# Optimization experiments

Hardware: AMD Instinct MI355X
Metric: run time of the kernel (lower is better)

## Reference

```python
import jax, jax.numpy as jnp
import numpy as np

THRESHOLD = 0.5
NEG_POS_RATIO = 3
ALPHA = 1.0
B, A, C, M = 128, 8732, 21, 8


def cxcy_to_xy(c):
    return jnp.concatenate([c[:, :2] - c[:, 2:] / 2.0, c[:, :2] + c[:, 2:] / 2.0], axis=1)


def cxcy_to_gcxgcy(cxcy, priors):
    g_cxcy = (cxcy[:, :2] - priors[:, :2]) / (priors[:, 2:] / 10.0)
    g_wh = jnp.log(cxcy[:, 2:] / priors[:, 2:]) * 5.0
    return jnp.concatenate([g_cxcy, g_wh], axis=1)


def find_jaccard_overlap(a, b):
    # a: [M,4] xy, b: [A,4] xy -> IoU [M,A]
    lt = jnp.maximum(a[:, None, :2], b[None, :, :2])
    rb = jnp.minimum(a[:, None, 2:], b[None, :, 2:])
    wh = jnp.clip(rb - lt, 0.0)
    inter = wh[..., 0] * wh[..., 1]
    area_a = (a[:, 2] - a[:, 0]) * (a[:, 3] - a[:, 1])
    area_b = (b[:, 2] - b[:, 0]) * (b[:, 3] - b[:, 1])
    return inter / (area_a[:, None] + area_b[None, :] - inter)


def setup_inputs() -> dict:
    key = jax.random.key(0)
    k1, k2, k3, k4, k5, k6 = jax.random.split(key, 6)
    predicted_locs = jax.random.normal(k1, (B, A, 4), dtype=jnp.float32)
    predicted_scores = jax.random.normal(k2, (B, A, C), dtype=jnp.float32)
    # ground-truth boxes in xy pixel coords within [0, 300], guaranteed x2>x1, y2>y1
    u = jax.random.uniform(k3, (B, M, 4), dtype=jnp.float32)
    x1y1 = u[..., :2] * 150.0
    x2y2 = x1y1 + u[..., 2:] * 140.0 + 10.0
    boxes = jnp.concatenate([x1y1, x2y2], axis=-1)
    labels = jax.random.randint(k4, (B, M), 1, C)  # 1..20, never background
    # anchor boxes in cxcy, w/h strictly positive
    cxcy = jax.random.uniform(k5, (A, 2), dtype=jnp.float32)
    wh = 0.05 + 0.95 * jax.random.uniform(k6, (A, 2), dtype=jnp.float32)
    anchor_boxes = jnp.concatenate([cxcy, wh], axis=1)
    return {"predicted_locs": predicted_locs, "predicted_scores": predicted_scores,
            "boxes": boxes, "labels": labels, "anchor_boxes": anchor_boxes}


def _match(boxes_i, labels_i, anchors_cxcy, anchors_xy):
    # boxes_i: [M,4] xy pixels, labels_i: [M]
    scaled = boxes_i / 300.0
    iou = find_jaccard_overlap(scaled, anchors_xy)            # [M, A]
    obj_for_anchor = jnp.argmax(iou, axis=0)                  # [A]
    iou_for_anchor = jnp.max(iou, axis=0)                     # [A]
    anchor_for_obj = jnp.argmax(iou, axis=1)                  # [M]
    obj_for_anchor = obj_for_anchor.at[anchor_for_obj].set(jnp.arange(M))
    iou_for_anchor = iou_for_anchor.at[anchor_for_obj].set(1.0)
    label_for_anchor = labels_i[obj_for_anchor]               # [A]
    label_for_anchor = jnp.where(iou_for_anchor < THRESHOLD, 0, label_for_anchor)
    true_locs = cxcy_to_gcxgcy(boxes_i[obj_for_anchor], anchors_cxcy)  # [A,4]
    return label_for_anchor, true_locs


def reference(predicted_locs, predicted_scores, boxes, labels, anchor_boxes):
    anchors_xy = cxcy_to_xy(anchor_boxes)
    true_classes, true_locs = jax.vmap(_match, in_axes=(0, 0, None, None))(
        boxes, labels, anchor_boxes, anchors_xy)              # [B,A], [B,A,4]

    pos = true_classes != 0                                   # [B,A]
    n_pos = pos.sum(axis=1)                                   # [B]
    n_pos_total = n_pos.sum()

    # L1Loss(mean) over positive anchors' 4 coords
    l1 = jnp.abs(predicted_locs - true_locs)                  # [B,A,4]
    loc_loss = (l1 * pos[..., None]).sum() / (n_pos_total.astype(jnp.float32) * 4.0)

    # per-anchor cross entropy
    logp = jax.nn.log_softmax(predicted_scores, axis=-1)      # [B,A,C]
    ce = -jnp.take_along_axis(logp, true_classes[..., None], axis=-1)[..., 0]  # [B,A]

    conf_pos = (ce * pos).sum()
    ce_neg = jnp.where(pos, 0.0, ce)
    ce_neg_sorted = -jnp.sort(-ce_neg, axis=1)                # descending per row
    ranks = jnp.arange(A)[None, :]
    hard = ranks < (NEG_POS_RATIO * n_pos)[:, None]
    conf_hard_neg = (ce_neg_sorted * hard).sum()

    conf_loss = (conf_hard_neg + conf_pos) / n_pos_total.astype(jnp.float32)
    return conf_loss + ALPHA * loc_loss
```

## Files before the change

kernel.cpp:

```cpp
#include <hip/hip_runtime.h>
#include <hip/hip_bf16.h>

constexpr int B = 128;
constexpr int A = 8732;
constexpr int C = 21;
constexpr int M = 8;

__global__ void k_init(float* accf, int* npt) {
    int t = threadIdx.x;
    if (t < 3) accf[t] = 0.f;
    if (t == 3) *npt = 0;
}

__global__ __launch_bounds__(1024) void k_match(
    const float* __restrict__ boxes,
    const int*   __restrict__ labels,
    const float* __restrict__ anchors,
    int*         __restrict__ packed,
    int*         __restrict__ n_pos,
    int*         __restrict__ npt)
{
    __shared__ float         s_iou[A];
    __shared__ unsigned char s_obj[A];
    __shared__ float s_pv[M][16];
    __shared__ int   s_pi[M][16];
    __shared__ int   s_force[M];
    __shared__ int   s_c[16];
    __shared__ float s_box[M][4];
    __shared__ int   s_lab[M];

    const int b = blockIdx.x;
    const int t = threadIdx.x;
    const int lane = t & 63;
    const int wv   = t >> 6;

    if (t < M * 4) ((float*)s_box)[t] = boxes[b * M * 4 + t];
    if (t < M)     s_lab[t] = labels[b * M + t];
    __syncthreads();

    float bb[M][4], barea[M];
#pragma unroll
    for (int m = 0; m < M; m++) {
        bb[m][0] = s_box[m][0] / 300.f;
        bb[m][1] = s_box[m][1] / 300.f;
        bb[m][2] = s_box[m][2] / 300.f;
        bb[m][3] = s_box[m][3] / 300.f;
        barea[m] = (bb[m][2] - bb[m][0]) * (bb[m][3] - bb[m][1]);
    }

    float bestv[M];
    int   besti[M];
#pragma unroll
    for (int m = 0; m < M; m++) { bestv[m] = -1.f; besti[m] = 0; }

    const float4* anch4 = (const float4*)anchors;
    for (int a = t; a < A; a += 1024) {
        float4 an = anch4[a];
        float ax1 = an.x - an.z / 2.0f, ay1 = an.y - an.w / 2.0f;
        float ax2 = an.x + an.z / 2.0f, ay2 = an.y + an.w / 2.0f;
        float aarea = (ax2 - ax1) * (ay2 - ay1);

        float bmax = -1.f; int bm = 0;
#pragma unroll
        for (int m = 0; m < M; m++) {
            float lx = fmaxf(bb[m][0], ax1), ly = fmaxf(bb[m][1], ay1);
            float rx = fminf(bb[m][2], ax2), ry = fminf(bb[m][3], ay2);
            float iw = fmaxf(rx - lx, 0.f), ih = fmaxf(ry - ly, 0.f);
            float inter = iw * ih;
            float iou = inter / (barea[m] + aarea - inter);
            if (iou > bmax) { bmax = iou; bm = m; }
            if (iou > bestv[m]) { bestv[m] = iou; besti[m] = a; }
        }
        s_iou[a] = bmax;
        s_obj[a] = (unsigned char)bm;
    }

#pragma unroll
    for (int m = 0; m < M; m++) {
        float v = bestv[m]; int i = besti[m];
        for (int off = 32; off > 0; off >>= 1) {
            float ov = __shfl_down(v, off);
            int   oi = __shfl_down(i, off);
            if (ov > v || (ov == v && oi < i)) { v = ov; i = oi; }
        }
        if (lane == 0) { s_pv[m][wv] = v; s_pi[m][wv] = i; }
    }
    __syncthreads();

    if (t < M) {
        float bv = -1.f; int bi = 0x7fffffff;
#pragma unroll
        for (int w = 0; w < 16; w++) {
            float v = s_pv[t][w]; int i = s_pi[t][w];
            if (v > bv || (v == bv && i < bi)) { bv = v; bi = i; }
        }
        s_force[t] = bi;
    }
    __syncthreads();

    if (t == 0) {
        for (int m = 0; m < M; m++) {
            int a = s_force[m];
            s_obj[a] = (unsigned char)m;
            s_iou[a] = 1.0f;
        }
    }
    __syncthreads();

    int cnt = 0;
    for (int a = t; a < A; a += 1024) {
        int obj = s_obj[a];
        int lab = s_lab[obj];
        if (s_iou[a] < 0.5f) lab = 0;
        packed[(size_t)b * A + a] = lab | (obj << 8);
        if (lab != 0) cnt++;
    }
    for (int off = 32; off > 0; off >>= 1) cnt += __shfl_down(cnt, off);
    if (lane == 0) s_c[wv] = cnt;
    __syncthreads();
    if (t == 0) {
        int c0 = 0;
#pragma unroll
        for (int w = 0; w < 16; w++) c0 += s_c[w];
        n_pos[b] = c0;
        atomicAdd(npt, c0);
    }
}

__global__ __launch_bounds__(256) void k_ce(
    const float* __restrict__ plocs,
    const float* __restrict__ pscores,
    const float* __restrict__ boxes,
    const float* __restrict__ anchors,
    int*         __restrict__ buf,
    float*       __restrict__ accf)
{
    constexpr int NQ = B * A / 4;
    const int i4 = blockIdx.x * 256 + threadIdx.x;
    float l_pos = 0.f, l_loc = 0.f;

    if (i4 < NQ) {
        const int base = i4 * 4;
        const float4* s4 = (const float4*)(pscores + (size_t)base * C);
        float4 v[21];
#pragma unroll
        for (int i = 0; i < 21; i++) v[i] = s4[i];
        const float* f = (const float*)v;

        int4 pk4 = ((const int4*)buf)[i4];
        const int pks[4] = {pk4.x, pk4.y, pk4.z, pk4.w};

        const int b = base / A;
        const int a0 = base - b * A;

        float4 cn4;
        float* cn = (float*)&cn4;
#pragma unroll
        for (int j = 0; j < 4; j++) {
            const float* row = f + j * C;
            const int lab = pks[j] & 255;
            const int obj = pks[j] >> 8;

            float mx = row[0];
#pragma unroll
            for (int c = 1; c < C; c++) mx = fmaxf(mx, row[c]);
            float sum = 0.f, slab = 0.f;
#pragma unroll
            for (int c = 0; c < C; c++) {
                sum += __expf(row[c] - mx);
                if (c == lab) slab = row[c];
            }
            float ce = mx + __logf(sum) - slab;

            cn[j] = ce;
            if (lab != 0) {
                cn[j] = 0.f;
                l_pos += ce;
                const float* bx = boxes + ((size_t)b * M + obj) * 4;
                const float* an = anchors + (size_t)(a0 + j) * 4;
                float dx = (bx[0] - an[0]) / (an[2] / 10.f);
                float dy = (bx[1] - an[1]) / (an[3] / 10.f);
                float dw = logf(bx[2] / an[2]) * 5.f;
                float dh = logf(bx[3] / an[3]) * 5.f;
                float4 p = ((const float4*)plocs)[base + j];
                l_loc += fabsf(p.x - dx) + fabsf(p.y - dy) +
                         fabsf(p.z - dw) + fabsf(p.w - dh);
            }
        }
        ((float4*)buf)[i4] = cn4;
    }

    for (int off = 32; off > 0; off >>= 1) {
        l_pos += __shfl_down(l_pos, off);
        l_loc += __shfl_down(l_loc, off);
    }
    if ((threadIdx.x & 63) == 0 && (l_pos != 0.f || l_loc != 0.f)) {
        atomicAdd(&accf[0], l_pos);
        atomicAdd(&accf[1], l_loc);
    }
}

__global__ __launch_bounds__(1024) void k_topk(
    const float* __restrict__ ce_neg,
    const int*   __restrict__ n_pos,
    float*       __restrict__ accf)
{
    __shared__ unsigned int vals[A];
    __shared__ unsigned int hist[256];
    __shared__ unsigned int s_prefix, s_krem;
    __shared__ float        rs[16];
    __shared__ unsigned int rc[16];

    const int b = blockIdx.x;
    const int t = threadIdx.x;
    const int lane = t & 63;
    const int wv   = t >> 6;
    const int K = 3 * n_pos[b];
    const float* row = ce_neg + (size_t)b * A;

    {
        const uint4* r4 = (const uint4*)row;
        uint4* v4 = (uint4*)vals;
        for (int i = t; i < A / 4; i += 1024) v4[i] = r4[i];
    }
    if (t == 0) { s_prefix = 0u; s_krem = (unsigned)K; }
    __syncthreads();

    if (K <= 0) return;

    if (K >= A) {
        float s = 0.f;
        for (int i = t; i < A; i += 1024) s += __uint_as_float(vals[i]);
        for (int off = 32; off > 0; off >>= 1) s += __shfl_down(s, off);
        if (lane == 0) rs[wv] = s;
        __syncthreads();
        if (t == 0) {
            float tot = 0.f;
#pragma unroll
            for (int w = 0; w < 16; w++) tot += rs[w];
            atomicAdd(&accf[2], tot);
        }
        return;
    }

    for (int pass = 0; pass < 4; pass++) {
        const int shift = 24 - 8 * pass;
        const unsigned pref = s_prefix;
        const unsigned krem = s_krem;
        if (t < 256) hist[t] = 0u;
        __syncthreads();
        for (int i = t; i < A; i += 1024) {
            unsigned int v = vals[i];
            if (pass == 0 || (v >> (shift + 8)) == pref)
                atomicAdd(&hist[(v >> shift) & 255u], 1u);
        }
        __syncthreads();
        if (t < 64) {
            unsigned h0 = hist[4 * t + 0], h1 = hist[4 * t + 1];
            unsigned h2 = hist[4 * t + 2], h3 = hist[4 * t + 3];
            unsigned s3 = h3, s2 = h2 + s3, s1 = h1 + s2, s0 = h0 + s1;
            unsigned suf = s0;
            for (int off = 1; off < 64; off <<= 1) {
                unsigned o = __shfl_down(suf, off);
                if (t + off < 64) suf += o;
            }
            unsigned above = suf - s0;
            hist[4 * t + 0] = above + s0;
            hist[4 * t + 1] = above + s1;
            hist[4 * t + 2] = above + s2;
            hist[4 * t + 3] = above + s3;
        }
        __syncthreads();
        if (t < 256) {
            unsigned ssT = hist[t];
            unsigned ssN = (t < 255) ? hist[t + 1] : 0u;
            if (ssT >= krem && ssN < krem) {
                s_prefix = (pref << 8) | (unsigned)t;
                s_krem   = krem - ssN;
            }
        }
        __syncthreads();
    }

    const unsigned int tb = s_prefix;
    float sg = 0.f; unsigned int cg = 0;
    for (int i = t; i < A; i += 1024) {
        unsigned int v = vals[i];
        if (v > tb) { sg += __uint_as_float(v); cg++; }
    }
    for (int off = 32; off > 0; off >>= 1) {
        sg += __shfl_down(sg, off);
        cg += __shfl_down(cg, off);
    }
    if (lane == 0) { rs[wv] = sg; rc[wv] = cg; }
    __syncthreads();
    if (t == 0) {
        float tv = __uint_as_float(tb);
        float tot = 0.f; unsigned cnt = 0;
#pragma unroll
        for (int w = 0; w < 16; w++) { tot += rs[w]; cnt += rc[w]; }
        atomicAdd(&accf[2], tot + (float)(K - (int)cnt) * tv);
    }
}

__global__ void k_final(const float* __restrict__ accf,
                        const int* __restrict__ npt,
                        float* __restrict__ out)
{
    float n = (float)(*npt);
    float conf_loss = (accf[2] + accf[0]) / n;
    float loc_loss  = accf[1] / (n * 4.f);
    out[0] = conf_loss + loc_loss;
}

extern "C" void kernel_launch(void* const* d_in, const int* in_sizes, int n_in,
                              void* d_out, int out_size, void* d_ws, size_t ws_size,
                              hipStream_t stream)
{
    const float* plocs   = (const float*)d_in[0];
    const float* pscores = (const float*)d_in[1];
    const float* boxes   = (const float*)d_in[2];
    const int*   labels  = (const int*)d_in[3];
    const float* anchors = (const float*)d_in[4];
    float*       out     = (float*)d_out;

    float* accf  = (float*)d_ws;
    int*   npt   = (int*)d_ws + 3;
    int*   n_pos = (int*)d_ws + 8;
    int*   buf   = (int*)d_ws + 8 + B;

    k_init<<<1, 64, 0, stream>>>(accf, npt);
    k_match<<<B, 1024, 0, stream>>>(boxes, labels, anchors, buf, n_pos, npt);
    constexpr int NQ = B * A / 4;
    k_ce<<<(NQ + 255) / 256, 256, 0, stream>>>(plocs, pscores, boxes, anchors, buf, accf);
    k_topk<<<B, 1024, 0, stream>>>((const float*)buf, n_pos, accf);
    k_final<<<1, 1, 0, stream>>>(accf, npt, out);
}
```

Measured before the change: 287.8 us.

## Split anchor matching across slices and stage CE scores through double-buffered LDS

Matching now runs as 16 slices per image with 256-thread blocks instead of one 1024-thread block per image. Each slice writes its packed labels directly and publishes per-object best anchors through 64-bit atomicMax keys. A new small patch kernel then applies the forced matches and corrects the positive counts. The CE kernel becomes a persistent grid that streams 256-anchor chunks of scores with coalesced float4 loads into a double-buffered shared-memory tile, prefetching the next chunk while it computes. This trades an extra launch and global atomics for much higher parallelism in matching and better load coalescing in CE.

```diff
diff --git a/kernel.cpp b/kernel.cpp
--- a/kernel.cpp
+++ b/kernel.cpp
@@ -1,38 +1,51 @@
 #include <hip/hip_runtime.h>
-#include <hip/hip_bf16.h>
 
 constexpr int B = 128;
 constexpr int A = 8732;
 constexpr int C = 21;
 constexpr int M = 8;
-
-__global__ void k_init(float* accf, int* npt) {
+constexpr int S  = 16;
+constexpr int AS = (A + S - 1) / S;
+constexpr int CH = 256;
+constexpr int NCH = B * A / CH;
+constexpr int CE_GRID = 768;
+
+
+__global__ __launch_bounds__(256) void k_init(float* accf, int* npt, int* n_pos,
+                                              unsigned long long* keys) {
     int t = threadIdx.x;
     if (t < 3) accf[t] = 0.f;
     if (t == 3) *npt = 0;
-}
-
-__global__ __launch_bounds__(1024) void k_match(
+    if (t < B) n_pos[t] = 0;
+#pragma unroll
+    for (int k = 0; k < (B * M + 255) / 256; k++) {
+        int i = t + k * 256;
+        if (i < B * M) keys[i] = 0ull;
+    }
+}
+
+__global__ __launch_bounds__(256) void k_match_slice(
     const float* __restrict__ boxes,
     const int*   __restrict__ labels,
     const float* __restrict__ anchors,
     int*         __restrict__ packed,
     int*         __restrict__ n_pos,
-    int*         __restrict__ npt)
-{
-    __shared__ float         s_iou[A];
-    __shared__ unsigned char s_obj[A];
-    __shared__ float s_pv[M][16];
-    __shared__ int   s_pi[M][16];
-    __shared__ int   s_force[M];
-    __shared__ int   s_c[16];
+    unsigned long long* __restrict__ keys)
+{
     __shared__ float s_box[M][4];
     __shared__ int   s_lab[M];
-
-    const int b = blockIdx.x;
-    const int t = threadIdx.x;
+    __shared__ float s_pv[M][4];
+    __shared__ int   s_pi[M][4];
+    __shared__ int   s_c[4];
+
+    const int bs = blockIdx.x;
+    const int b  = bs >> 4;
+    const int s  = bs & (S - 1);
+    const int t  = threadIdx.x;
     const int lane = t & 63;
     const int wv   = t >> 6;
+    const int a_lo = s * AS;
+    const int a_hi = (a_lo + AS < A) ? a_lo + AS : A;
 
     if (t < M * 4) ((float*)s_box)[t] = boxes[b * M * 4 + t];
     if (t < M)     s_lab[t] = labels[b * M + t];
@@ -51,10 +64,11 @@
     float bestv[M];
     int   besti[M];
 #pragma unroll
-    for (int m = 0; m < M; m++) { bestv[m] = -1.f; besti[m] = 0; }
+    for (int m = 0; m < M; m++) { bestv[m] = -1.f; besti[m] = a_lo; }
 
     const float4* anch4 = (const float4*)anchors;
-    for (int a = t; a < A; a += 1024) {
+    int cnt = 0;
+    for (int a = a_lo + t; a < a_hi; a += 256) {
         float4 an = anch4[a];
         float ax1 = an.x - an.z / 2.0f, ay1 = an.y - an.w / 2.0f;
         float ax2 = an.x + an.z / 2.0f, ay2 = an.y + an.w / 2.0f;
@@ -71,8 +85,10 @@
             if (iou > bmax) { bmax = iou; bm = m; }
             if (iou > bestv[m]) { bestv[m] = iou; besti[m] = a; }
         }
-        s_iou[a] = bmax;
-        s_obj[a] = (unsigned char)bm;
+        int lab = s_lab[bm];
+        if (bmax < 0.5f) lab = 0;
+        packed[(size_t)b * A + a] = lab | (bm << 8);
+        if (lab != 0) cnt++;
     }
 
 #pragma unroll
@@ -85,45 +101,52 @@
         }
         if (lane == 0) { s_pv[m][wv] = v; s_pi[m][wv] = i; }
     }
+    for (int off = 32; off > 0; off >>= 1) cnt += __shfl_down(cnt, off);
+    if (lane == 0) s_c[wv] = cnt;
     __syncthreads();
 
     if (t < M) {
         float bv = -1.f; int bi = 0x7fffffff;
 #pragma unroll
-        for (int w = 0; w < 16; w++) {
+        for (int w = 0; w < 4; w++) {
             float v = s_pv[t][w]; int i = s_pi[t][w];
             if (v > bv || (v == bv && i < bi)) { bv = v; bi = i; }
         }
-        s_force[t] = bi;
-    }
-    __syncthreads();
-
+        unsigned long long key =
+            ((unsigned long long)__float_as_uint(bv) << 32) |
+            (unsigned long long)(0xFFFFFFFFu - (unsigned)bi);
+        atomicMax(&keys[b * M + t], key);
+    }
+    if (t == 0) atomicAdd(&n_pos[b], s_c[0] + s_c[1] + s_c[2] + s_c[3]);
+}
+
+__global__ __launch_bounds__(64) void k_patch(
+    const int* __restrict__ labels,
+    const unsigned long long* __restrict__ keys,
+    int* __restrict__ packed,
+    int* __restrict__ n_pos,
+    int* __restrict__ npt)
+{
+    __shared__ int s_force[M];
+    const int b = blockIdx.x;
+    const int t = threadIdx.x;
+    if (t < M) {
+        unsigned long long k = keys[b * M + t];
+        s_force[t] = (int)(0xFFFFFFFFu - (unsigned)(k & 0xFFFFFFFFull));
+    }
+    __syncthreads();
     if (t == 0) {
+        int delta = 0;
         for (int m = 0; m < M; m++) {
             int a = s_force[m];
-            s_obj[a] = (unsigned char)m;
-            s_iou[a] = 1.0f;
-        }
-    }
-    __syncthreads();
-
-    int cnt = 0;
-    for (int a = t; a < A; a += 1024) {
-        int obj = s_obj[a];
-        int lab = s_lab[obj];
-        if (s_iou[a] < 0.5f) lab = 0;
-        packed[(size_t)b * A + a] = lab | (obj << 8);
-        if (lab != 0) cnt++;
-    }
-    for (int off = 32; off > 0; off >>= 1) cnt += __shfl_down(cnt, off);
-    if (lane == 0) s_c[wv] = cnt;
-    __syncthreads();
-    if (t == 0) {
-        int c0 = 0;
-#pragma unroll
-        for (int w = 0; w < 16; w++) c0 += s_c[w];
-        n_pos[b] = c0;
-        atomicAdd(npt, c0);
+            int prev = packed[(size_t)b * A + a];
+            int newlab = labels[b * M + m];
+            packed[(size_t)b * A + a] = newlab | (m << 8);
+            delta += (newlab != 0 ? 1 : 0) - ((prev & 255) != 0 ? 1 : 0);
+        }
+        int rc = n_pos[b] + delta;
+        n_pos[b] = rc;
+        atomicAdd(npt, rc);
     }
 }
 
@@ -135,68 +158,90 @@
     int*         __restrict__ buf,
     float*       __restrict__ accf)
 {
-    constexpr int NQ = B * A / 4;
-    const int i4 = blockIdx.x * 256 + threadIdx.x;
-    float l_pos = 0.f, l_loc = 0.f;
-
-    if (i4 < NQ) {
-        const int base = i4 * 4;
-        const float4* s4 = (const float4*)(pscores + (size_t)base * C);
-        float4 v[21];
-#pragma unroll
-        for (int i = 0; i < 21; i++) v[i] = s4[i];
-        const float* f = (const float*)v;
-
-        int4 pk4 = ((const int4*)buf)[i4];
-        const int pks[4] = {pk4.x, pk4.y, pk4.z, pk4.w};
-
-        const int b = base / A;
-        const int a0 = base - b * A;
-
-        float4 cn4;
-        float* cn = (float*)&cn4;
-#pragma unroll
-        for (int j = 0; j < 4; j++) {
-            const float* row = f + j * C;
-            const int lab = pks[j] & 255;
-            const int obj = pks[j] >> 8;
-
-            float mx = row[0];
-#pragma unroll
-            for (int c = 1; c < C; c++) mx = fmaxf(mx, row[c]);
+    __shared__ float s_sc[2][CH * C];
+    const int t = threadIdx.x;
+
+    int c = blockIdx.x;
+    float4 r[6];
+    int pk;
+    {
+        const float4* src = (const float4*)(pscores + (size_t)c * CH * C);
+#pragma unroll
+        for (int k = 0; k < 5; k++) r[k] = src[t + k * 256];
+        if (t < 64) r[5] = src[t + 1280];
+        pk = buf[c * CH + t];
+    }
+
+    int p = 0;
+    while (true) {
+        {
+            float4* dst = (float4*)s_sc[p];
+#pragma unroll
+            for (int k = 0; k < 5; k++) dst[t + k * 256] = r[k];
+            if (t < 64) dst[t + 1280] = r[5];
+        }
+        __syncthreads();
+
+        const int cnext = c + CE_GRID;
+        const bool more = cnext < NCH;
+        int pk_next = 0;
+        if (more) {
+            const float4* src = (const float4*)(pscores + (size_t)cnext * CH * C);
+#pragma unroll
+            for (int k = 0; k < 5; k++) r[k] = src[t + k * 256];
+            if (t < 64) r[5] = src[t + 1280];
+            pk_next = buf[cnext * CH + t];
+        }
+
+        {
+            const int idx = c * CH + t;
+            const int lab = pk & 255;
+            const int obj = pk >> 8;
+            const float* row = s_sc[p] + t * C;
+            float v[C];
+            float mx = -1e30f;
+#pragma unroll
+            for (int i = 0; i < C; i++) { v[i] = row[i]; mx = fmaxf(mx, v[i]); }
             float sum = 0.f, slab = 0.f;
 #pragma unroll
-            for (int c = 0; c < C; c++) {
-                sum += __expf(row[c] - mx);
-                if (c == lab) slab = row[c];
+            for (int i = 0; i < C; i++) {
+                sum += __expf(v[i] - mx);
+                if (i == lab) slab = v[i];
             }
             float ce = mx + __logf(sum) - slab;
 
-            cn[j] = ce;
+            float l_pos = 0.f, l_loc = 0.f;
+            float cn = ce;
             if (lab != 0) {
-                cn[j] = 0.f;
-                l_pos += ce;
+                cn = 0.f;
+                l_pos = ce;
+                int b = idx / A;
+                int a = idx - b * A;
                 const float* bx = boxes + ((size_t)b * M + obj) * 4;
-                const float* an = anchors + (size_t)(a0 + j) * 4;
+                const float* an = anchors + (size_t)a * 4;
                 float dx = (bx[0] - an[0]) / (an[2] / 10.f);
                 float dy = (bx[1] - an[1]) / (an[3] / 10.f);
                 float dw = logf(bx[2] / an[2]) * 5.f;
                 float dh = logf(bx[3] / an[3]) * 5.f;
-                float4 p = ((const float4*)plocs)[base + j];
-                l_loc += fabsf(p.x - dx) + fabsf(p.y - dy) +
-                         fabsf(p.z - dw) + fabsf(p.w - dh);
-            }
-        }
-        ((float4*)buf)[i4] = cn4;
-    }
-
-    for (int off = 32; off > 0; off >>= 1) {
-        l_pos += __shfl_down(l_pos, off);
-        l_loc += __shfl_down(l_loc, off);
-    }
-    if ((threadIdx.x & 63) == 0 && (l_pos != 0.f || l_loc != 0.f)) {
-        atomicAdd(&accf[0], l_pos);
-        atomicAdd(&accf[1], l_loc);
+                float4 pl = ((const float4*)plocs)[idx];
+                l_loc = fabsf(pl.x - dx) + fabsf(pl.y - dy) +
+                        fabsf(pl.z - dw) + fabsf(pl.w - dh);
+            }
+            ((float*)buf)[idx] = cn;
+
+            for (int off = 32; off > 0; off >>= 1) {
+                l_pos += __shfl_down(l_pos, off);
+                l_loc += __shfl_down(l_loc, off);
+            }
+            if ((t & 63) == 0 && (l_pos != 0.f || l_loc != 0.f)) {
+                atomicAdd(&accf[0], l_pos);
+                atomicAdd(&accf[1], l_loc);
+            }
+        }
+
+        if (!more) break;
+        c = cnext; pk = pk_next; p ^= 1;
+        __syncthreads();
     }
 }
 
@@ -327,12 +372,13 @@
     float* accf  = (float*)d_ws;
     int*   npt   = (int*)d_ws + 3;
     int*   n_pos = (int*)d_ws + 8;
-    int*   buf   = (int*)d_ws + 8 + B;
-
-    k_init<<<1, 64, 0, stream>>>(accf, npt);
-    k_match<<<B, 1024, 0, stream>>>(boxes, labels, anchors, buf, n_pos, npt);
-    constexpr int NQ = B * A / 4;
-    k_ce<<<(NQ + 255) / 256, 256, 0, stream>>>(plocs, pscores, boxes, anchors, buf, accf);
+    unsigned long long* keys = (unsigned long long*)((int*)d_ws + 136);
+    int*   buf   = (int*)d_ws + 136 + 2 * B * M;
+
+    k_init<<<1, 256, 0, stream>>>(accf, npt, n_pos, keys);
+    k_match_slice<<<B * S, 256, 0, stream>>>(boxes, labels, anchors, buf, n_pos, keys);
+    k_patch<<<B, 64, 0, stream>>>(labels, keys, buf, n_pos, npt);
+    k_ce<<<CE_GRID, 256, 0, stream>>>(plocs, pscores, boxes, anchors, buf, accf);
     k_topk<<<B, 1024, 0, stream>>>((const float*)buf, n_pos, accf);
     k_final<<<1, 1, 0, stream>>>(accf, npt, out);
 }
```

Result: slower. 446.6 us (+55.2%).
